# Optimization experiments

Measured on AMD Instinct MI355X. Metric: run time of the kernel, lower is better.

## Reference

```python
import jax, jax.numpy as jnp
import numpy as np

N, NCB, DIM, CB_SIZE = 16384, 8, 32, 1024


def setup_inputs() -> dict:
    key = jax.random.key(0)
    k1, k2, k3 = jax.random.split(key, 3)
    x = jax.random.normal(k1, (N, NCB, DIM), dtype=jnp.float32)
    codebook = jax.random.normal(k2, (NCB, CB_SIZE, DIM), dtype=jnp.float32)
    rate_bias = jax.random.normal(k3, (NCB, CB_SIZE), dtype=jnp.float32)
    return {"x": x, "codebook": codebook, "rate_bias": rate_bias}


def reference(x, codebook, rate_bias):
    # x: (N, ncb, dim), codebook: (ncb, cb_size, dim)
    x_sq = jnp.sum(x * x, axis=-1, keepdims=True)            # (N, ncb, 1)
    cb_sq = jnp.sum(codebook * codebook, axis=-1)            # (ncb, cb_size)
    cross = jnp.einsum('nkd,kcd->nkc', x, codebook)          # (N, ncb, cb_size)
    dist = x_sq + cb_sq - 2.0 * cross                        # (N, ncb, cb_size)
    dist = dist + rate_bias                                  # rate_bias broadcast
    index = jnp.argmin(dist, axis=-1, keepdims=True)         # (N, ncb, 1)
    one_hot = jax.nn.one_hot(index[..., 0], CB_SIZE, dtype=dist.dtype)  # (N, ncb, cb_size)
    x_hat = jnp.einsum('nkc,kcd->nkd', one_hot, codebook)    # (N, ncb, dim)
    return (x_hat, one_hot, index)
```

## Files before the change

### kernel.cpp

```cpp
#include <hip/hip_runtime.h>

typedef float f32x2 __attribute__((ext_vector_type(2)));
typedef float f32x4 __attribute__((ext_vector_type(4)));

#define NN 16384
#define NCB 8
#define DIM 32
#define CB 1024
#define RPB 512
#define QC 256
#define TILE 32
#define NTL (QC / TILE)

__device__ __forceinline__ void gload_lds16(const void* g, void* l) {
    __builtin_amdgcn_global_load_lds(
        (const __attribute__((address_space(1))) unsigned int*)g,
        (__attribute__((address_space(3))) unsigned int*)l, 16, 0, 0);
}

__device__ __forceinline__ f32x2 pkfma(f32x2 a, f32x2 b, f32x2 c) {
    f32x2 d = c;
    asm("v_pk_fma_f32 %0, %1, %2, %0" : "+v"(d) : "v"(a), "v"(b));
    return d;
}

__global__ __launch_bounds__(256) void vq_csq(const float* __restrict__ cb,
                                              const float* __restrict__ rb,
                                              float* __restrict__ out) {
    int i = blockIdx.x * 256 + threadIdx.x;
    if (i >= NCB * CB) return;
    const float4* c4 = reinterpret_cast<const float4*>(cb + (size_t)i * DIM);
    float s0 = 0.f, s1 = 0.f, s2 = 0.f, s3 = 0.f;
#pragma unroll
    for (int j = 0; j < 8; ++j) {
        float4 v = c4[j];
        s0 = fmaf(v.x, v.x, s0);
        s1 = fmaf(v.y, v.y, s1);
        s2 = fmaf(v.z, v.z, s2);
        s3 = fmaf(v.w, v.w, s3);
    }
    out[i] = ((s0 + s1) + (s2 + s3)) + rb[i];
}

__global__ __launch_bounds__(512, 1) void vq_fused(
    const float* __restrict__ x, const float* __restrict__ cb,
    const float* __restrict__ csqb, float* __restrict__ xhat,
    float* __restrict__ onehot, float* __restrict__ idxf) {
    __shared__ f32x4 tiles[8][2][TILE * 8];
    __shared__ float pd[4][RPB];
    __shared__ int pi[4][RPB];

    const int tid = threadIdx.x;
    const int w = tid >> 6;
    const int lane = tid & 63;
    const int rh = w >> 2;
    const int q = w & 3;
    const int k = blockIdx.x & (NCB - 1);
    const int n0 = (blockIdx.x >> 3) * RPB;

    const f32x4* cbk4 =
        reinterpret_cast<const f32x4*>(cb + (size_t)k * CB * DIM);
    const float* cqk = csqb + (size_t)k * CB;

    const int rbase = rh * 256 + lane * 4;
    f32x2 xlo[4][8], xhi[4][8];
    float xsq[4];
#pragma unroll
    for (int j = 0; j < 4; ++j) {
        const int n = n0 + rbase + j;
        const f32x4* xp =
            reinterpret_cast<const f32x4*>(x + ((size_t)n * NCB + k) * DIM);
        f32x4 xt[8];
#pragma unroll
        for (int jj = 0; jj < 8; ++jj) xt[jj] = xp[jj];
        float q0 = 0.f, q1 = 0.f, q2 = 0.f, q3 = 0.f;
#pragma unroll
        for (int jj = 0; jj < 8; ++jj) {
            q0 = fmaf(xt[jj].x, xt[jj].x, q0);
            q1 = fmaf(xt[jj].y, xt[jj].y, q1);
            q2 = fmaf(xt[jj].z, xt[jj].z, q2);
            q3 = fmaf(xt[jj].w, xt[jj].w, q3);
        }
        xsq[j] = (q0 + q1) + (q2 + q3);
#pragma unroll
        for (int jj = 0; jj < 8; ++jj) {
            xlo[j][jj] = __builtin_shufflevector(xt[jj], xt[jj], 0, 1);
            xhi[j][jj] = __builtin_shufflevector(xt[jj], xt[jj], 2, 3);
        }
    }

    float best[4];
    int bi[4];
#pragma unroll
    for (int j = 0; j < 4; ++j) {
        best[j] = 3.4028235e38f;
        bi[j] = 0;
    }

    const int qbase = q * QC;
    float cqall[4];
#pragma unroll
    for (int i = 0; i < 4; ++i) cqall[i] = cqk[qbase + i * 64 + lane];

    __builtin_amdgcn_sched_barrier(0);
#pragma unroll
    for (int i = 0; i < 4; ++i)
        gload_lds16(cbk4 + (size_t)qbase * 8 + i * 64 + lane,
                    &tiles[w][0][i * 64]);
    __builtin_amdgcn_sched_barrier(0);

    float4* oh4 = reinterpret_cast<float4*>(onehot);
    const float4 z4 = make_float4(0.f, 0.f, 0.f, 0.f);

#pragma unroll
    for (int th = 0; th < 4; ++th) {
        const float cql = cqall[th];
        for (int sub = 0; sub < 2; ++sub) {
            const int t = th * 2 + sub;
            const int b = t & 1;

            {
                const int zb = n0 + w * 64 + t * 8;
#pragma unroll
                for (int rr = 0; rr < 8; ++rr) {
                    float4* rp = oh4 + ((size_t)(zb + rr) * NCB + k) * 256;
#pragma unroll
                    for (int s = 0; s < 4; ++s) rp[s * 64 + lane] = z4;
                }
            }
            __builtin_amdgcn_sched_barrier(0);

            if (t < NTL - 1) {
#pragma unroll
                for (int i = 0; i < 4; ++i)
                    gload_lds16(
                        cbk4 + ((size_t)qbase + (t + 1) * TILE) * 8 + i * 64 +
                            lane,
                        &tiles[w][b ^ 1][i * 64]);
                __builtin_amdgcn_sched_barrier(0);
                asm volatile("s_waitcnt vmcnt(36)" ::: "memory");
            } else {
                asm volatile("s_waitcnt vmcnt(32)" ::: "memory");
            }
            __builtin_amdgcn_sched_barrier(0);

            const f32x4* buf = &tiles[w][b][0];
#pragma unroll 2
            for (int c = 0; c < TILE; ++c) {
                const float cqv = __int_as_float(__builtin_amdgcn_readlane(
                    __float_as_int(cql), (sub << 5) + c));
                f32x4 A[8];
#pragma unroll
                for (int jj = 0; jj < 8; ++jj) A[jj] = buf[c * 8 + jj];
                const int cg = qbase + t * TILE + c;

#pragma unroll
                for (int j = 0; j < 4; ++j) {
                    f32x2 acc01 = {0.f, 0.f}, acc23 = {0.f, 0.f};
#pragma unroll
                    for (int jj = 0; jj < 8; ++jj) {
                        const f32x2 alo =
                            __builtin_shufflevector(A[jj], A[jj], 0, 1);
                        const f32x2 ahi =
                            __builtin_shufflevector(A[jj], A[jj], 2, 3);
                        acc01 = pkfma(xlo[j][jj], alo, acc01);
                        acc23 = pkfma(xhi[j][jj], ahi, acc23);
                    }
                    const float dot =
                        (acc01.x + acc01.y) + (acc23.x + acc23.y);
                    const float dist = fmaf(-2.f, dot, xsq[j] + cqv);
                    if (dist < best[j]) {
                        best[j] = dist;
                        bi[j] = cg;
                    }
                }
            }
        }
    }

#pragma unroll
    for (int j = 0; j < 4; ++j) {
        pd[q][rbase + j] = best[j];
        pi[q][rbase + j] = bi[j];
    }
    __syncthreads();

    {
        const int r = tid;
        float bd = pd[0][r];
        int bx = pi[0][r];
#pragma unroll
        for (int qq = 1; qq < 4; ++qq) {
            const float dq = pd[qq][r];
            const int iq = pi[qq][r];
            if (dq < bd) {
                bd = dq;
                bx = iq;
            }
        }
        const int n = n0 + r;
        idxf[(size_t)n * NCB + k] = (float)bx;
        const f32x4* src = cbk4 + (size_t)bx * 8;
        f32x4* dst =
            reinterpret_cast<f32x4*>(xhat + ((size_t)n * NCB + k) * DIM);
#pragma unroll
        for (int jj = 0; jj < 8; ++jj) dst[jj] = src[jj];
        onehot[((size_t)n * NCB + k) * CB + bx] = 1.0f;
    }
}

extern "C" void kernel_launch(void* const* d_in, const int* in_sizes, int n_in,
                              void* d_out, int out_size, void* d_ws,
                              size_t ws_size, hipStream_t stream) {
    const float* x = (const float*)d_in[0];
    const float* cb = (const float*)d_in[1];
    const float* rb = (const float*)d_in[2];

    float* out = (float*)d_out;
    float* xhat = out;
    float* onehot = out + (size_t)NN * NCB * DIM;
    float* idxf = onehot + (size_t)NN * NCB * CB;

    float* csqb = (float*)d_ws;

    vq_csq<<<(NCB * CB + 255) / 256, 256, 0, stream>>>(cb, rb, csqb);
    vq_fused<<<(NN / RPB) * NCB, 512, 0, stream>>>(x, cb, csqb, xhat, onehot,
                                                   idxf);
}
```

Baseline: 175.4 us.

## Stage full codebook slice in LDS once and interleave onehot zeroing per code

```diff
diff --git a/kernel.cpp b/kernel.cpp
--- a/kernel.cpp
+++ b/kernel.cpp
@@ -8,9 +8,6 @@
 #define DIM 32
 #define CB 1024
 #define RPB 512
-#define QC 256
-#define TILE 32
-#define NTL (QC / TILE)
 
 __device__ __forceinline__ void gload_lds16(const void* g, void* l) {
     __builtin_amdgcn_global_load_lds(
@@ -42,11 +39,11 @@
     out[i] = ((s0 + s1) + (s2 + s3)) + rb[i];
 }
 
-__global__ __launch_bounds__(512, 1) void vq_fused(
+__global__ __launch_bounds__(512, 2) void vq_fused(
     const float* __restrict__ x, const float* __restrict__ cb,
     const float* __restrict__ csqb, float* __restrict__ xhat,
     float* __restrict__ onehot, float* __restrict__ idxf) {
-    __shared__ f32x4 tiles[8][2][TILE * 8];
+    __shared__ f32x4 cbL[CB * 8];
     __shared__ float pd[4][RPB];
     __shared__ int pi[4][RPB];
 
@@ -62,6 +59,10 @@
         reinterpret_cast<const f32x4*>(cb + (size_t)k * CB * DIM);
     const float* cqk = csqb + (size_t)k * CB;
 
+#pragma unroll
+    for (int j = 0; j < 16; ++j)
+        gload_lds16(cbk4 + j * 512 + tid, &cbL[j * 512 + tid]);
+
     const int rbase = rh * 256 + lane * 4;
     f32x2 xlo[4][8], xhi[4][8];
     float xsq[4];
@@ -89,6 +90,13 @@
         }
     }
 
+    const int qbase = q * 256;
+    float cqall[4];
+#pragma unroll
+    for (int i = 0; i < 4; ++i) cqall[i] = cqk[qbase + i * 64 + lane];
+
+    __syncthreads();
+
     float best[4];
     int bi[4];
 #pragma unroll
@@ -97,82 +105,61 @@
         bi[j] = 0;
     }
 
-    const int qbase = q * QC;
-    float cqall[4];
-#pragma unroll
-    for (int i = 0; i < 4; ++i) cqall[i] = cqk[qbase + i * 64 + lane];
-
-    __builtin_amdgcn_sched_barrier(0);
-#pragma unroll
-    for (int i = 0; i < 4; ++i)
-        gload_lds16(cbk4 + (size_t)qbase * 8 + i * 64 + lane,
-                    &tiles[w][0][i * 64]);
-    __builtin_amdgcn_sched_barrier(0);
-
     float4* oh4 = reinterpret_cast<float4*>(onehot);
     const float4 z4 = make_float4(0.f, 0.f, 0.f, 0.f);
 
 #pragma unroll
-    for (int th = 0; th < 4; ++th) {
-        const float cql = cqall[th];
-        for (int sub = 0; sub < 2; ++sub) {
-            const int t = th * 2 + sub;
-            const int b = t & 1;
+    for (int g = 0; g < 4; ++g) {
+        const float cql = cqall[g];
+#pragma unroll 2
+        for (int cc = 0; cc < 64; ++cc) {
+            const int ce = g * 64 + cc;
+            const int c = qbase + ce;
 
             {
-                const int zb = n0 + w * 64 + t * 8;
-#pragma unroll
-                for (int rr = 0; rr < 8; ++rr) {
-                    float4* rp = oh4 + ((size_t)(zb + rr) * NCB + k) * 256;
-#pragma unroll
-                    for (int s = 0; s < 4; ++s) rp[s * 64 + lane] = z4;
+                const int zrow = n0 + w * 64 + (ce >> 2);
+                oh4[((size_t)zrow * NCB + k) * 256 + (ce & 3) * 64 + lane] = z4;
+            }
+
+            const float cqv = __int_as_float(
+                __builtin_amdgcn_readlane(__float_as_int(cql), cc));
+
+            f32x2 acc01[4], acc23[4];
+#pragma unroll
+            for (int j = 0; j < 4; ++j) {
+                acc01[j] = (f32x2){0.f, 0.f};
+                acc23[j] = (f32x2){0.f, 0.f};
+            }
+#pragma unroll
+            for (int jj = 0; jj < 4; ++jj) {
+                const f32x4 A = cbL[(size_t)c * 8 + jj];
+                const f32x2 alo = __builtin_shufflevector(A, A, 0, 1);
+                const f32x2 ahi = __builtin_shufflevector(A, A, 2, 3);
+#pragma unroll
+                for (int j = 0; j < 4; ++j) {
+                    acc01[j] = pkfma(xlo[j][jj], alo, acc01[j]);
+                    acc23[j] = pkfma(xhi[j][jj], ahi, acc23[j]);
                 }
             }
-            __builtin_amdgcn_sched_barrier(0);
-
-            if (t < NTL - 1) {
-#pragma unroll
-                for (int i = 0; i < 4; ++i)
-                    gload_lds16(
-                        cbk4 + ((size_t)qbase + (t + 1) * TILE) * 8 + i * 64 +
-                            lane,
-                        &tiles[w][b ^ 1][i * 64]);
-                __builtin_amdgcn_sched_barrier(0);
-                asm volatile("s_waitcnt vmcnt(36)" ::: "memory");
-            } else {
-                asm volatile("s_waitcnt vmcnt(32)" ::: "memory");
-            }
-            __builtin_amdgcn_sched_barrier(0);
-
-            const f32x4* buf = &tiles[w][b][0];
-#pragma unroll 2
-            for (int c = 0; c < TILE; ++c) {
-                const float cqv = __int_as_float(__builtin_amdgcn_readlane(
-                    __float_as_int(cql), (sub << 5) + c));
-                f32x4 A[8];
-#pragma unroll
-                for (int jj = 0; jj < 8; ++jj) A[jj] = buf[c * 8 + jj];
-                const int cg = qbase + t * TILE + c;
-
+#pragma unroll
+            for (int jj = 4; jj < 8; ++jj) {
+                const f32x4 A = cbL[(size_t)c * 8 + jj];
+                const f32x2 alo = __builtin_shufflevector(A, A, 0, 1);
+                const f32x2 ahi = __builtin_shufflevector(A, A, 2, 3);
 #pragma unroll
                 for (int j = 0; j < 4; ++j) {
-                    f32x2 acc01 = {0.f, 0.f}, acc23 = {0.f, 0.f};
-#pragma unroll
-                    for (int jj = 0; jj < 8; ++jj) {
-                        const f32x2 alo =
-                            __builtin_shufflevector(A[jj], A[jj], 0, 1);
-                        const f32x2 ahi =
-                            __builtin_shufflevector(A[jj], A[jj], 2, 3);
-                        acc01 = pkfma(xlo[j][jj], alo, acc01);
-                        acc23 = pkfma(xhi[j][jj], ahi, acc23);
-                    }
-                    const float dot =
-                        (acc01.x + acc01.y) + (acc23.x + acc23.y);
-                    const float dist = fmaf(-2.f, dot, xsq[j] + cqv);
-                    if (dist < best[j]) {
-                        best[j] = dist;
-                        bi[j] = cg;
-                    }
+                    acc01[j] = pkfma(xlo[j][jj], alo, acc01[j]);
+                    acc23[j] = pkfma(xhi[j][jj], ahi, acc23[j]);
+                }
+            }
+#pragma unroll
+            for (int j = 0; j < 4; ++j) {
+                const float dot =
+                    (acc01[j].x + acc01[j].y) + (acc23[j].x + acc23[j].y);
+                const float dist = fmaf(-2.f, dot, xsq[j] + cqv);
+                if (dist < best[j]) {
+                    best[j] = dist;
+                    bi[j] = c;
                 }
             }
         }
```

New measurement: 189.2 us. +7.8%, slower.
